# Performance work log

Measured on AMD Instinct MI355X. Metric: run time of the kernel, lower is better.

The kernel has to match this reference:

```python
import jax, jax.numpy as jnp
import numpy as np

N_BINS = 64
INPUT_DIM = 8
R = 1.2
BOUND = 10.0
BETA = 1e-06
N = 2097152


def _mesh_and_elmt():
    m = N_BINS / 2
    idx = jnp.arange(N_BINS + 1, dtype=jnp.float32) - m
    x1L = BOUND * (R - 1.0) / (R ** m - 1.0)
    xr = (1.0 - R ** jnp.abs(idx)) / (1.0 - R)
    xr = jnp.where(idx >= 0, x1L * xr, -x1L * xr)
    xr = (xr + BOUND) / (2.0 * BOUND)
    mesh = jnp.concatenate([jnp.zeros((1,), jnp.float32), xr[1:-1], jnp.ones((1,), jnp.float32)])  # [n_bins+1]
    elmt = mesh[1:] - mesh[:-1]  # [n_bins]
    return mesh, elmt


def _pdf_normalize(p, elmt):
    # pdf: [n_bins+1, d]; F_ref: [n_bins, d] cumulative bin integrals
    p0 = jnp.full((1, INPUT_DIM), BETA, jnp.float32)
    ep = jnp.exp(p)
    px = ep * ((elmt[:-1] + elmt[1:]) / 2.0)[:, None]
    scale = (1.0 - (elmt[0] + elmt[-1]) * BETA / 2.0) / jnp.sum(px, 0, keepdims=True)
    px = scale * ep
    pdf = jnp.concatenate([p0, px, p0], 0)
    cell = (pdf[:-1] + pdf[1:]) / 2.0 * elmt[:, None]  # [n_bins, d]
    F_ref = jnp.concatenate([jnp.zeros((1, INPUT_DIM), jnp.float32),
                             jnp.cumsum(cell, 0)[:N_BINS - 1]], 0)
    return pdf, F_ref


def setup_inputs() -> dict:
    key = jax.random.key(0)
    k1, k2 = jax.random.split(key)
    x = jax.random.normal(k1, (N, INPUT_DIM), dtype=jnp.float32)
    logdet = jnp.zeros((N, 1), dtype=jnp.float32)
    p = jax.random.normal(k2, (N_BINS - 1, INPUT_DIM), dtype=jnp.float32)
    return {"x": x, "logdet": logdet, "p": p}


def reference(x, logdet, p):
    mesh, elmt = _mesh_and_elmt()
    pdf, F_ref = _pdf_normalize(p, elmt)

    xs = (x + BOUND) / (2.0 * BOUND)  # [N, d] in [0,1] for covered points
    k = jnp.searchsorted(mesh, xs, side='right') - 1  # [N, d]
    cover = (k >= 0) & (k <= N_BINS - 1)
    k = jnp.clip(k, 0, N_BINS - 1)
    col = jnp.arange(INPUT_DIM)[None, :]

    v1 = pdf[k, col]            # [N, d]
    v2 = pdf[k + 1, col]
    xm = xs - mesh[k]
    h = elmt[k]
    F_pre = F_ref[k, col]

    y = jnp.where(cover, F_pre + xm * xm / 2.0 * (v2 - v1) / h + xm * v1, xs)
    dld = jnp.where(cover, xm * (v2 - v1) / h + v1, 1.0)
    logdet = logdet + jnp.sum(jnp.log(dld), -1, keepdims=True)

    y = y * 2.0 * BOUND - BOUND
    y = jnp.where(y > BOUND, BETA * (y - BOUND) + BOUND, y)
    logdet = logdet + jnp.sum(jnp.log(jnp.where(y > BOUND, BETA, 1.0)), -1, keepdims=True)
    y = jnp.where(y < -BOUND, BETA * (y + BOUND) - BOUND, y)
    logdet = logdet + jnp.sum(jnp.log(jnp.where(y < -BOUND, BETA, 1.0)), -1, keepdims=True)
    return y, logdet
```

## Files before the change

kernel.cpp:

```cpp
#include <hip/hip_runtime.h>
#include <math.h>

#define NDIM   8
#define NBINS  64
#define LOG_BETA   (-13.815510557964274f)
#define LN2F       0.69314718055994531f
#define ALPHA      34.0821892f
#define INV_LOG2R  3.80178401692393f
#define L2R        0.26303440583379378f

typedef float f32x4 __attribute__((ext_vector_type(4)));

__global__ __launch_bounds__(256, 6) void cdfq_fused(const float* __restrict__ x,
                                                     const float* __restrict__ logdet_in,
                                                     const float* __restrict__ p,
                                                     float* __restrict__ y_out,
                                                     float* __restrict__ ld_out,
                                                     int n)
{
    __shared__ float4 stbl[NDIM * NBINS];

    const int t  = threadIdx.x;
    const int T  = gridDim.x * blockDim.x;
    const int i0 = blockIdx.x * blockDim.x + t;
    const int iters = n / T;
    const bool fast = (iters == 4);
    const float4* xv4 = (const float4*)x;

    float4 Xa[4], Xb[4]; float Ld[4];
    if (fast) {
#pragma unroll
        for (int j = 0; j < 4; ++j) {
            int g = i0 + j * T;
            Xa[j] = xv4[2 * g];
            Xb[j] = xv4[2 * g + 1];
            Ld[j] = logdet_in[g];
        }
    }
    __builtin_amdgcn_sched_barrier(0);

    {
        const int lane = t & 63;
        const int w    = t >> 6;
        const float pw32 = exp2f(32.0f * L2R);
        const float inv  = 0.5f / (pw32 - 1.0f);
        auto meshf = [&](float tt) {
            float fidx = tt - 32.0f;
            float pw = exp2f(fabsf(fidx) * L2R);
            float r  = (pw - 1.0f) * inv;
            return 0.5f + ((fidx >= 0.0f) ? r : -r);
        };
        const float m0  = meshf((float)lane);
        const float m1  = meshf((float)(lane + 1));
        const float el  = m1 - m0;
        const float el1 = __shfl_down(el, 1);
        const float e0e63 = 2.0f * (meshf(1.0f) - meshf(0.0f));

#pragma unroll
        for (int dd = 0; dd < 2; ++dd) {
            const int d = 2 * w + dd;
            float ep = 0.0f;
            if (lane < 63) ep = __expf(p[lane * NDIM + d]);
            float s = ep * 0.5f * (el + el1);
#pragma unroll
            for (int off = 32; off; off >>= 1) s += __shfl_xor(s, off);
            const float scale = (1.0f - e0e63 * 5e-7f) / s;
            const float epu = __shfl_up(ep, 1);
            const float pdl = (lane == 0)  ? 1e-6f : scale * epu;
            const float pdn = (lane == 63) ? 1e-6f : scale * ep;
            const float cell = 0.5f * (pdl + pdn) * el;
            float v = cell;
#pragma unroll
            for (int off = 1; off < 64; off <<= 1) {
                float u = __shfl_up(v, off);
                if (lane >= off) v += u;
            }
            stbl[(d << 6) | lane] = make_float4(pdl, (pdn - pdl) / el, v - cell, m0);
        }
    }
    __syncthreads();

    auto body8 = [&](float4 A, float4 B, float Lin, int q) {
        float xd[8] = {A.x, A.y, A.z, A.w, B.x, B.y, B.z, B.w};
        float yd[8], dd8[8];
        float extra = 0.0f;

#pragma unroll
        for (int d = 0; d < 8; ++d) {
            float xo = xd[d];
            float xs = fmaf(xo, 0.05f, 0.5f);
            float gg = __log2f(fmaf(ALPHA, fabsf(xo), 1.0f)) * INV_LOG2R;
            int jf = (int)fminf(gg, 31.0f);
            int k  = (xo >= 0.0f) ? (32 + jf) : (31 - jf);

            float4 tb = stbl[(d << 6) + k];
            float xm  = xs - tb.w;
            bool cov  = (xs >= 0.0f) && (xs < 1.0f);

            float yc = tb.z + xm * fmaf(0.5f * xm, tb.y, tb.x);
            float dv = fmaf(xm, tb.y, tb.x);
            float yy = cov ? yc : xs;
            dd8[d]   = cov ? dv : 1.0f;

            yy = fmaf(yy, 20.0f, -10.0f);
            if (yy > 10.0f)  { yy = fmaf(1e-6f, yy - 10.0f, 10.0f);  extra += LOG_BETA; }
            if (yy < -10.0f) { yy = fmaf(1e-6f, yy + 10.0f, -10.0f); extra += LOG_BETA; }
            yd[d] = yy;
        }

        float q1 = (dd8[0] * dd8[1]) * (dd8[2] * dd8[3]);
        float q2 = (dd8[4] * dd8[5]) * (dd8[6] * dd8[7]);
        float contrib = fmaf(__log2f(q1) + __log2f(q2), LN2F, extra);

        f32x4 y1 = { yd[0], yd[1], yd[2], yd[3] };
        f32x4 y2 = { yd[4], yd[5], yd[6], yd[7] };
        __builtin_nontemporal_store(y1, (f32x4*)y_out + 2 * q);
        __builtin_nontemporal_store(y2, (f32x4*)y_out + 2 * q + 1);
        __builtin_nontemporal_store(Lin + contrib, ld_out + q);
    };

    if (fast) {
#pragma unroll
        for (int j = 0; j < 4; ++j)
            body8(Xa[j], Xb[j], Ld[j], i0 + j * T);
        for (int g = i0 + 4 * T; g < n; g += T)
            body8(xv4[2 * g], xv4[2 * g + 1], logdet_in[g], g);
    } else {
        for (int g = i0; g < n; g += T)
            body8(xv4[2 * g], xv4[2 * g + 1], logdet_in[g], g);
    }
}

extern "C" void kernel_launch(void* const* d_in, const int* in_sizes, int n_in,
                              void* d_out, int out_size, void* d_ws, size_t ws_size,
                              hipStream_t stream) {
    const float* x      = (const float*)d_in[0];
    const float* logdet = (const float*)d_in[1];
    const float* p      = (const float*)d_in[2];

    const int n = in_sizes[1];
    float* y_out  = (float*)d_out;
    float* ld_out = (float*)d_out + (size_t)n * NDIM;

    const int block = 256;
    int grid = 2048;
    if ((long long)grid * block > (long long)n) grid = (n + block - 1) / block;
    cdfq_fused<<<grid, block, 0, stream>>>(x, logdet, p, y_out, ld_out, n);
}
```

Baseline: 146.4 us.

## Replace upfront 4-deep prefetch with rolling one-ahead prefetch loop

Instead of loading all four iterations' inputs into registers before building the table, the kernel now loads only the first row and then prefetches the next row while computing the current one. This cuts register pressure, and launch bounds rise to 8 blocks per CU for more occupancy. It also simplifies bin-index computation using XOR, a coverage test on |x|, and running products instead of arrays. The catch is less memory-level parallelism per thread: only one row is in flight instead of four, so more waves must cover the latency.

```diff
diff --git a/kernel.cpp b/kernel.cpp
--- a/kernel.cpp
+++ b/kernel.cpp
@@ -11,7 +11,7 @@
 
 typedef float f32x4 __attribute__((ext_vector_type(4)));
 
-__global__ __launch_bounds__(256, 6) void cdfq_fused(const float* __restrict__ x,
+__global__ __launch_bounds__(256, 8) void cdfq_fused(const float* __restrict__ x,
                                                      const float* __restrict__ logdet_in,
                                                      const float* __restrict__ p,
                                                      float* __restrict__ y_out,
@@ -24,19 +24,10 @@
     const int T  = gridDim.x * blockDim.x;
     const int i0 = blockIdx.x * blockDim.x + t;
     const int iters = n / T;
-    const bool fast = (iters == 4);
-    const float4* xv4 = (const float4*)x;
+    const f32x4* xv4 = (const f32x4*)x;
 
-    float4 Xa[4], Xb[4]; float Ld[4];
-    if (fast) {
-#pragma unroll
-        for (int j = 0; j < 4; ++j) {
-            int g = i0 + j * T;
-            Xa[j] = xv4[2 * g];
-            Xb[j] = xv4[2 * g + 1];
-            Ld[j] = logdet_in[g];
-        }
-    }
+    f32x4 A0, B0; float L0;
+    if (iters > 0) { A0 = xv4[2 * i0]; B0 = xv4[2 * i0 + 1]; L0 = logdet_in[i0]; }
     __builtin_amdgcn_sched_barrier(0);
 
     {
@@ -80,27 +71,28 @@
     }
     __syncthreads();
 
-    auto body8 = [&](float4 A, float4 B, float Lin, int q) {
-        float xd[8] = {A.x, A.y, A.z, A.w, B.x, B.y, B.z, B.w};
-        float yd[8], dd8[8];
+    auto body = [&](f32x4 A, f32x4 B, float Lin, int q) {
+        float yd[8];
+        float p0 = 1.0f, p1 = 1.0f;
         float extra = 0.0f;
 
 #pragma unroll
         for (int d = 0; d < 8; ++d) {
-            float xo = xd[d];
+            float xo = (d < 4) ? A[d] : B[d - 4];
             float xs = fmaf(xo, 0.05f, 0.5f);
             float gg = __log2f(fmaf(ALPHA, fabsf(xo), 1.0f)) * INV_LOG2R;
             int jf = (int)fminf(gg, 31.0f);
-            int k  = (xo >= 0.0f) ? (32 + jf) : (31 - jf);
+            int k  = ((xo >= 0.0f) ? 32 : 31) ^ jf;
 
-            float4 tb = stbl[(d << 6) + k];
-            float xm  = xs - tb.w;
-            bool cov  = (xs >= 0.0f) && (xs < 1.0f);
+            f32x4 tv = *(const f32x4*)&stbl[(d << 6) + k];
+            float xm = xs - tv[3];
+            bool cov = (fabsf(xo) < 10.0f);
 
-            float yc = tb.z + xm * fmaf(0.5f * xm, tb.y, tb.x);
-            float dv = fmaf(xm, tb.y, tb.x);
+            float yc = fmaf(xm, fmaf(0.5f * xm, tv[1], tv[0]), tv[2]);
+            float dv = fmaf(xm, tv[1], tv[0]);
             float yy = cov ? yc : xs;
-            dd8[d]   = cov ? dv : 1.0f;
+            float dl = cov ? dv : 1.0f;
+            if (d & 4) p1 *= dl; else p0 *= dl;
 
             yy = fmaf(yy, 20.0f, -10.0f);
             if (yy > 10.0f)  { yy = fmaf(1e-6f, yy - 10.0f, 10.0f);  extra += LOG_BETA; }
@@ -108,9 +100,7 @@
             yd[d] = yy;
         }
 
-        float q1 = (dd8[0] * dd8[1]) * (dd8[2] * dd8[3]);
-        float q2 = (dd8[4] * dd8[5]) * (dd8[6] * dd8[7]);
-        float contrib = fmaf(__log2f(q1) + __log2f(q2), LN2F, extra);
+        float contrib = fmaf(__log2f(p0) + __log2f(p1), LN2F, extra);
 
         f32x4 y1 = { yd[0], yd[1], yd[2], yd[3] };
         f32x4 y2 = { yd[4], yd[5], yd[6], yd[7] };
@@ -119,16 +109,24 @@
         __builtin_nontemporal_store(Lin + contrib, ld_out + q);
     };
 
-    if (fast) {
-#pragma unroll
-        for (int j = 0; j < 4; ++j)
-            body8(Xa[j], Xb[j], Ld[j], i0 + j * T);
-        for (int g = i0 + 4 * T; g < n; g += T)
-            body8(xv4[2 * g], xv4[2 * g + 1], logdet_in[g], g);
-    } else {
-        for (int g = i0; g < n; g += T)
-            body8(xv4[2 * g], xv4[2 * g + 1], logdet_in[g], g);
+    for (int j = 0; j < iters; ++j) {
+        f32x4 An, Bn; float Ln;
+        const bool more = (j + 1 < iters);
+        if (more) {
+            int qn = i0 + (j + 1) * T;
+            An = xv4[2 * qn];
+            Bn = xv4[2 * qn + 1];
+            Ln = logdet_in[qn];
+        }
+        __builtin_amdgcn_sched_barrier(0);
+
+        body(A0, B0, L0, i0 + j * T);
+
+        if (more) { A0 = An; B0 = Bn; L0 = Ln; }
     }
+
+    for (int q = i0 + iters * T; q < n; q += T)
+        body(xv4[2 * q], xv4[2 * q + 1], logdet_in[q], q);
 }
 
 extern "C" void kernel_launch(void* const* d_in, const int* in_sizes, int n_in,
```

Result: faster. 140.0 us (-4.4%).
